# Performance work log

Measured on AMD Instinct MI355X. Metric: run time of the kernel, lower is better.

Reference implementation:

```python
import jax, jax.numpy as jnp
import numpy as np

H = 1024
NH = 16
HD = H // NH  # 64

def setup_inputs() -> dict:
    key = jax.random.key(0)
    ks = jax.random.split(key, 6)
    B, S = 2, 2048
    hidden_states = jax.random.normal(ks[0], (B, S, H), dtype=jnp.float32)
    attention_mask = jnp.ones((B, S), dtype=jnp.int32)
    sc = 1.0 / np.sqrt(H)
    Wq = jax.random.normal(ks[1], (H, H), dtype=jnp.float32) * sc
    Wk = jax.random.normal(ks[2], (H, H), dtype=jnp.float32) * sc
    Wv = jax.random.normal(ks[3], (H, H), dtype=jnp.float32) * sc
    Wo = jax.random.normal(ks[4], (H, H), dtype=jnp.float32) * sc
    return {"hidden_states": hidden_states, "attention_mask": attention_mask,
            "Wq": Wq, "Wk": Wk, "Wv": Wv, "Wo": Wo}

def reference(hidden_states, attention_mask, Wq, Wk, Wv, Wo):
    B, S, _ = hidden_states.shape
    # nn.Linear(bias=False): y = x @ W.T
    q = hidden_states @ Wq.T
    k = hidden_states @ Wk.T
    v = hidden_states @ Wv.T
    # [B, NH, S, HD]
    q = q.reshape(B, S, NH, HD).transpose(0, 2, 1, 3)
    k = k.reshape(B, S, NH, HD).transpose(0, 2, 1, 3)
    v = v.reshape(B, S, NH, HD).transpose(0, 2, 1, 3)
    # ELU+1 feature map
    q = jax.nn.elu(q) + 1.0
    k = jax.nn.elu(k) + 1.0
    # [B, NH, S, S]
    attn = jnp.einsum('bhqd,bhkd->bhqk', q, k)
    mask = attention_mask[:, None, None, :]  # [B,1,1,S]
    attn = jnp.where(mask == 0, -jnp.inf, attn)
    attn = jax.nn.softmax(attn, axis=-1)
    # dropout p=0.0 (eval) -> identity
    out = jnp.einsum('bhqk,bhkd->bhqd', attn, v)
    out = out.transpose(0, 2, 1, 3).reshape(B, S, H)
    return out @ Wo.T
```

## Files before the change

kernel.cpp:

```cpp
#include <hip/hip_runtime.h>

#define H_ 1024
#define NH_ 16
#define HD_ 64
#define B_ 2
#define S_ 2048
#define BS_ 4096

typedef _Float16 half8 __attribute__((ext_vector_type(8)));
typedef _Float16 half4_t __attribute__((ext_vector_type(4)));
typedef float floatx4 __attribute__((ext_vector_type(4)));

#define LOG2E 1.44269504088896f

__device__ __forceinline__ void async_copy16(void* lds, const void* g) {
  __builtin_amdgcn_global_load_lds(
      (const __attribute__((address_space(1))) unsigned int*)g,
      (__attribute__((address_space(3))) unsigned int*)lds, 16, 0, 0);
}

__global__ __launch_bounds__(256) void cvt_all(
    const float* __restrict__ hs, const float* __restrict__ wq,
    const float* __restrict__ wk, const float* __restrict__ wv,
    const float* __restrict__ wo,
    _Float16* __restrict__ hs_h, _Float16* __restrict__ w_h) {
  int i = blockIdx.x * 256 + threadIdx.x;
  int idx = i * 4;
  const float* src; _Float16* dst; int off;
  if (idx < BS_ * H_) {
    src = hs; dst = hs_h; off = idx;
  } else {
    int j = idx - BS_ * H_;
    int w = j >> 20;
    off = j & ((1 << 20) - 1);
    src = (w == 0) ? wq : (w == 1) ? wk : (w == 2) ? wv : wo;
    dst = w_h + (size_t)w * (H_ * H_);
  }
  float4 f = *(const float4*)(src + off);
  half4_t o;
  o.x = (_Float16)f.x; o.y = (_Float16)f.y;
  o.z = (_Float16)f.z; o.w = (_Float16)f.w;
  *(half4_t*)(dst + off) = o;
}

__global__ __launch_bounds__(256) void qkv_gemm(
    const _Float16* __restrict__ A, const _Float16* __restrict__ Wall,
    _Float16* __restrict__ qh, _Float16* __restrict__ kh,
    _Float16* __restrict__ vt) {
  const int z = blockIdx.z;
  const _Float16* W = Wall + (size_t)z * (H_ * H_);
  const int rbase = blockIdx.y * 128;
  const int cbase = blockIdx.x * 128;
  __shared__ _Float16 As[128 * 32];
  __shared__ _Float16 Bs[128 * 32];
  const int tid = threadIdx.x, lane = tid & 63, w = tid >> 6;
  const int quad = lane >> 4, l16 = lane & 15;
  const int wr = (w >> 1) * 64, wc = (w & 1) * 64;

  floatx4 zero = {0.f, 0.f, 0.f, 0.f};
  floatx4 acc[4][4];
#pragma unroll
  for (int i = 0; i < 4; ++i)
#pragma unroll
    for (int j = 0; j < 4; ++j) acc[i][j] = zero;

  const int srow = w * 32 + (lane >> 2);
  const int sseg = (lane & 3) * 8;
  const _Float16* Ag = A + (size_t)(rbase + srow) * H_ + sseg;
  const _Float16* Bg = W + (size_t)(cbase + srow) * H_ + sseg;

  for (int k0 = 0; k0 < H_; k0 += 32) {
    async_copy16(&As[(w * 32) * 32], Ag + k0);
    async_copy16(&As[(w * 32 + 16) * 32], Ag + 16 * H_ + k0);
    async_copy16(&Bs[(w * 32) * 32], Bg + k0);
    async_copy16(&Bs[(w * 32 + 16) * 32], Bg + 16 * H_ + k0);
    __syncthreads();
    half8 af[4], bf[4];
#pragma unroll
    for (int t = 0; t < 4; ++t)
      af[t] = *(half8*)&As[(wr + t * 16 + l16) * 32 + quad * 8];
#pragma unroll
    for (int t = 0; t < 4; ++t)
      bf[t] = *(half8*)&Bs[(wc + t * 16 + l16) * 32 + quad * 8];
#pragma unroll
    for (int i = 0; i < 4; ++i)
#pragma unroll
      for (int j = 0; j < 4; ++j)
        acc[i][j] = __builtin_amdgcn_mfma_f32_16x16x32_f16(af[i], bf[j],
                                                           acc[i][j], 0, 0, 0);
    __syncthreads();
  }
#pragma unroll
  for (int i = 0; i < 4; ++i) {
    int r0 = rbase + wr + i * 16 + quad * 4;
    int b = r0 >> 11, sl0 = r0 & (S_ - 1);
#pragma unroll
    for (int j = 0; j < 4; ++j) {
      int col = cbase + wc + j * 16 + l16;
      int h = col >> 6, d = col & 63;
      if (z == 2) {
        half4_t pk;
#pragma unroll
        for (int r = 0; r < 4; ++r) pk[r] = (_Float16)acc[i][j][r];
        *(half4_t*)&vt[((size_t)(b * NH_ + h) * HD_ + d) * S_ + sl0] = pk;
      } else {
        _Float16* outp = (z == 0) ? qh : kh;
        float scale = (z == 0) ? LOG2E : 1.0f;
#pragma unroll
        for (int r = 0; r < 4; ++r) {
          float x = acc[i][j][r];
          x = ((x > 0.f) ? (x + 1.f) : __expf(x)) * scale;
          outp[((size_t)(b * NH_ + h) * S_ + sl0 + r) * HD_ + d] = (_Float16)x;
        }
      }
    }
  }
}

__global__ __launch_bounds__(256, 2) void flash_attn(
    const _Float16* __restrict__ qh, const _Float16* __restrict__ kh,
    const _Float16* __restrict__ vt, const int* __restrict__ mask,
    _Float16* __restrict__ attn_out) {
  const int bh = blockIdx.y, b = bh >> 4, h = bh & 15;
  const int qbase = blockIdx.x * 128;
  const int tid = threadIdx.x, w = tid >> 6, lane = tid & 63;
  const int quad = lane >> 4, l16 = lane & 15;

  __shared__ _Float16 Kt[128 * 64];
  __shared__ _Float16 Vt[64 * 128];
  __shared__ _Float16 Pt[4][32 * 68];

  const _Float16* Q = qh + (size_t)bh * (S_ * HD_);
  const _Float16* K = kh + (size_t)bh * (S_ * HD_);
  const _Float16* Vg = vt + (size_t)bh * (HD_ * S_);
  const int* Mb = mask + b * S_;

  half8 qf[2][2];
#pragma unroll
  for (int g = 0; g < 2; ++g) {
    int qr = qbase + w * 32 + g * 16 + l16;
    qf[g][0] = *(const half8*)&Q[qr * 64 + quad * 8];
    qf[g][1] = *(const half8*)&Q[qr * 64 + 32 + quad * 8];
  }

  floatx4 zero = {0.f, 0.f, 0.f, 0.f};
  floatx4 o[2][4];
#pragma unroll
  for (int g = 0; g < 2; ++g)
#pragma unroll
    for (int i = 0; i < 4; ++i) o[g][i] = zero;
  float mi[2][4], li[2][4];
#pragma unroll
  for (int g = 0; g < 2; ++g)
#pragma unroll
    for (int r = 0; r < 4; ++r) { mi[g][r] = -3e38f; li[g][r] = 0.f; }

  const int krow_off = lane >> 3;
  const int kslot = lane & 7;
  const int kchunk = kslot ^ (krow_off & 7);
  const int vrow_off = lane >> 4;
  const int vslot = lane & 15;

  for (int kt = 0; kt < S_ / 128; ++kt) {
    const int key0 = kt * 128;
#pragma unroll
    for (int u = 0; u < 4; ++u) {
      int kl = w * 32 + u * 8;
      async_copy16(&Kt[kl * 64],
                   K + (size_t)(key0 + kl + krow_off) * 64 + kchunk * 8);
    }
#pragma unroll
    for (int u = 0; u < 4; ++u) {
      int d0 = w * 16 + u * 4 + vrow_off;
      int c0 = vslot ^ (d0 & 15);
      async_copy16(&Vt[(w * 16 + u * 4) * 128],
                   Vg + (size_t)d0 * S_ + key0 + c0 * 8);
    }
    int m0 = Mb[key0 + lane];
    int m1 = Mb[key0 + 64 + lane];
    __syncthreads();

    floatx4 sa[2][8];
#pragma unroll
    for (int g = 0; g < 2; ++g)
#pragma unroll
      for (int ct = 0; ct < 8; ++ct) sa[g][ct] = zero;
    {
      int s0 = quad ^ (l16 & 7);
      int s1 = (4 + quad) ^ (l16 & 7);
#pragma unroll
      for (int ct = 0; ct < 8; ++ct) {
        int key = ct * 16 + l16;
        half8 bf0 = *(half8*)&Kt[key * 64 + s0 * 8];
        half8 bf1 = *(half8*)&Kt[key * 64 + s1 * 8];
        sa[0][ct] = __builtin_amdgcn_mfma_f32_16x16x32_f16(qf[0][0], bf0, sa[0][ct], 0, 0, 0);
        sa[0][ct] = __builtin_amdgcn_mfma_f32_16x16x32_f16(qf[0][1], bf1, sa[0][ct], 0, 0, 0);
        sa[1][ct] = __builtin_amdgcn_mfma_f32_16x16x32_f16(qf[1][0], bf0, sa[1][ct], 0, 0, 0);
        sa[1][ct] = __builtin_amdgcn_mfma_f32_16x16x32_f16(qf[1][1], bf1, sa[1][ct], 0, 0, 0);
      }
    }
    if (__any((m0 == 0) || (m1 == 0))) {
#pragma unroll
      for (int ct = 0; ct < 8; ++ct) {
        if (Mb[key0 + ct * 16 + l16] == 0) {
#pragma unroll
          for (int g = 0; g < 2; ++g) {
            sa[g][ct][0] = -1e30f; sa[g][ct][1] = -1e30f;
            sa[g][ct][2] = -1e30f; sa[g][ct][3] = -1e30f;
          }
        }
      }
    }
#pragma unroll
    for (int g = 0; g < 2; ++g)
#pragma unroll
      for (int r = 0; r < 4; ++r) {
        float mx = sa[g][0][r];
#pragma unroll
        for (int ct = 1; ct < 8; ++ct) mx = fmaxf(mx, sa[g][ct][r]);
        mx = fmaxf(mx, __shfl_xor(mx, 1));
        mx = fmaxf(mx, __shfl_xor(mx, 2));
        mx = fmaxf(mx, __shfl_xor(mx, 4));
        mx = fmaxf(mx, __shfl_xor(mx, 8));
        float mn = fmaxf(mi[g][r], mx);
        float alpha = __builtin_amdgcn_exp2f(mi[g][r] - mn);
        mi[g][r] = mn;
        float rs = 0.f;
#pragma unroll
        for (int ct = 0; ct < 8; ++ct) {
          float p = __builtin_amdgcn_exp2f(sa[g][ct][r] - mn);
          sa[g][ct][r] = p;
          rs += p;
        }
        rs += __shfl_xor(rs, 1);
        rs += __shfl_xor(rs, 2);
        rs += __shfl_xor(rs, 4);
        rs += __shfl_xor(rs, 8);
        li[g][r] = li[g][r] * alpha + rs;
        o[g][0][r] *= alpha; o[g][1][r] *= alpha;
        o[g][2][r] *= alpha; o[g][3][r] *= alpha;
      }
#pragma unroll
    for (int hv = 0; hv < 2; ++hv) {
#pragma unroll
      for (int g = 0; g < 2; ++g)
#pragma unroll
        for (int c = 0; c < 4; ++c)
#pragma unroll
          for (int r = 0; r < 4; ++r)
            Pt[w][(g * 16 + quad * 4 + r) * 68 + c * 16 + l16] =
                (_Float16)sa[g][hv * 4 + c][r];
      __builtin_amdgcn_s_waitcnt(0xC07F);
#pragma unroll
      for (int kk2 = 0; kk2 < 2; ++kk2) {
        int kk = hv * 2 + kk2;
        half8 pf0 = *(half8*)&Pt[w][l16 * 68 + kk2 * 32 + quad * 8];
        half8 pf1 = *(half8*)&Pt[w][(16 + l16) * 68 + kk2 * 32 + quad * 8];
#pragma unroll
        for (int ct2 = 0; ct2 < 4; ++ct2) {
          int d = ct2 * 16 + l16;
          int vs = (kk * 4 + quad) ^ (l16 & 15);
          half8 vf = *(half8*)&Vt[d * 128 + vs * 8];
          o[0][ct2] = __builtin_amdgcn_mfma_f32_16x16x32_f16(pf0, vf, o[0][ct2], 0, 0, 0);
          o[1][ct2] = __builtin_amdgcn_mfma_f32_16x16x32_f16(pf1, vf, o[1][ct2], 0, 0, 0);
        }
      }
    }
    __syncthreads();
  }
#pragma unroll
  for (int g = 0; g < 2; ++g)
#pragma unroll
    for (int ct2 = 0; ct2 < 4; ++ct2)
#pragma unroll
      for (int r = 0; r < 4; ++r) {
        int row = qbase + w * 32 + g * 16 + quad * 4 + r;
        int d = ct2 * 16 + l16;
        float val = o[g][ct2][r] / li[g][r];
        attn_out[((size_t)(b * S_ + row)) * H_ + h * HD_ + d] = (_Float16)val;
      }
}

__global__ __launch_bounds__(256) void out_gemm(
    const _Float16* __restrict__ A, const _Float16* __restrict__ W,
    float* __restrict__ out) {
  const int rbase = blockIdx.y * 128;
  const int cbase = blockIdx.x * 64;
  __shared__ _Float16 As[128 * 32];
  __shared__ _Float16 Bs[64 * 32];
  const int tid = threadIdx.x, lane = tid & 63, w = tid >> 6;
  const int quad = lane >> 4, l16 = lane & 15;

  floatx4 zero = {0.f, 0.f, 0.f, 0.f};
  floatx4 acc[2][4];
#pragma unroll
  for (int i = 0; i < 2; ++i)
#pragma unroll
    for (int j = 0; j < 4; ++j) acc[i][j] = zero;

  const int srowA = w * 32 + (lane >> 2);
  const int srowB = w * 16 + (lane >> 2);
  const int sseg = (lane & 3) * 8;
  const _Float16* Ag = A + (size_t)(rbase + srowA) * H_ + sseg;
  const _Float16* Bg = W + (size_t)(cbase + srowB) * H_ + sseg;

  for (int k0 = 0; k0 < H_; k0 += 32) {
    async_copy16(&As[(w * 32) * 32], Ag + k0);
    async_copy16(&As[(w * 32 + 16) * 32], Ag + 16 * H_ + k0);
    async_copy16(&Bs[(w * 16) * 32], Bg + k0);
    __syncthreads();
    half8 af[2], bf[4];
#pragma unroll
    for (int t = 0; t < 2; ++t)
      af[t] = *(half8*)&As[(w * 32 + t * 16 + l16) * 32 + quad * 8];
#pragma unroll
    for (int t = 0; t < 4; ++t)
      bf[t] = *(half8*)&Bs[(t * 16 + l16) * 32 + quad * 8];
#pragma unroll
    for (int i = 0; i < 2; ++i)
#pragma unroll
      for (int j = 0; j < 4; ++j)
        acc[i][j] = __builtin_amdgcn_mfma_f32_16x16x32_f16(af[i], bf[j],
                                                           acc[i][j], 0, 0, 0);
    __syncthreads();
  }
#pragma unroll
  for (int i = 0; i < 2; ++i) {
    int r0 = rbase + w * 32 + i * 16 + quad * 4;
#pragma unroll
    for (int j = 0; j < 4; ++j) {
      int col = cbase + j * 16 + l16;
#pragma unroll
      for (int r = 0; r < 4; ++r)
        out[(size_t)(r0 + r) * H_ + col] = acc[i][j][r];
    }
  }
}

extern "C" void kernel_launch(void* const* d_in, const int* in_sizes, int n_in,
                              void* d_out, int out_size, void* d_ws,
                              size_t ws_size, hipStream_t stream) {
  const float* hs = (const float*)d_in[0];
  const int* mask = (const int*)d_in[1];
  const float* Wq = (const float*)d_in[2];
  const float* Wk = (const float*)d_in[3];
  const float* Wv = (const float*)d_in[4];
  const float* Wo = (const float*)d_in[5];
  float* out = (float*)d_out;

  _Float16* p = (_Float16*)d_ws;
  _Float16* hs_h = p; p += (size_t)BS_ * H_;
  _Float16* w_h = p;  p += (size_t)4 * H_ * H_;
  _Float16* q_h = p;  p += (size_t)BS_ * H_;
  _Float16* k_h = p;  p += (size_t)BS_ * H_;
  _Float16* v_t = p;  p += (size_t)BS_ * H_;
  _Float16* ao_h = p; p += (size_t)BS_ * H_;

  cvt_all<<<8192, 256, 0, stream>>>(hs, Wq, Wk, Wv, Wo, hs_h, w_h);
  qkv_gemm<<<dim3(8, 32, 3), 256, 0, stream>>>(hs_h, w_h, q_h, k_h, v_t);
  flash_attn<<<dim3(16, 32), 256, 0, stream>>>(q_h, k_h, v_t, mask, ao_h);
  out_gemm<<<dim3(16, 32), 256, 0, stream>>>(ao_h, w_h + (size_t)3 * H_ * H_, out);
}
```

Baseline: 213.9 us.

## Double-buffer K/V tiles and keep P in registers via transposed MFMA

The attention kernel now double-buffers K and V tiles in LDS, issuing the async load for the next tile before computing the current one, so there is one barrier per iteration. The QK^T MFMA operands are swapped so each lane holds a whole query row's scores. That lets the row max and sum use two cross-quad shuffles instead of four, and lets P be fed straight from registers into 16x16x16 MFMAs for PV, dropping the P round-trip through LDS. The output is written as packed half4 stores. The trade-off is twice the K/V LDS footprint, which may limit occupancy, and a smaller-K MFMA shape for the PV product.

New measurement: 192.7 us. 1.11x faster.

```diff
diff --git a/kernel.cpp b/kernel.cpp
--- a/kernel.cpp
+++ b/kernel.cpp
@@ -126,9 +126,8 @@
   const int tid = threadIdx.x, w = tid >> 6, lane = tid & 63;
   const int quad = lane >> 4, l16 = lane & 15;
 
-  __shared__ _Float16 Kt[128 * 64];
-  __shared__ _Float16 Vt[64 * 128];
-  __shared__ _Float16 Pt[4][32 * 68];
+  __shared__ _Float16 Kt[2][128 * 64];
+  __shared__ _Float16 Vt[2][64 * 128];
 
   const _Float16* Q = qh + (size_t)bh * (S_ * HD_);
   const _Float16* K = kh + (size_t)bh * (S_ * HD_);
@@ -149,11 +148,7 @@
   for (int g = 0; g < 2; ++g)
 #pragma unroll
     for (int i = 0; i < 4; ++i) o[g][i] = zero;
-  float mi[2][4], li[2][4];
-#pragma unroll
-  for (int g = 0; g < 2; ++g)
-#pragma unroll
-    for (int r = 0; r < 4; ++r) { mi[g][r] = -3e38f; li[g][r] = 0.f; }
+  float mi[2] = {-3e38f, -3e38f}, li[2] = {0.f, 0.f};
 
   const int krow_off = lane >> 3;
   const int kslot = lane & 7;
@@ -161,24 +156,45 @@
   const int vrow_off = lane >> 4;
   const int vslot = lane & 15;
 
-  for (int kt = 0; kt < S_ / 128; ++kt) {
-    const int key0 = kt * 128;
+  {
 #pragma unroll
     for (int u = 0; u < 4; ++u) {
       int kl = w * 32 + u * 8;
-      async_copy16(&Kt[kl * 64],
-                   K + (size_t)(key0 + kl + krow_off) * 64 + kchunk * 8);
+      async_copy16(&Kt[0][kl * 64], K + (size_t)(kl + krow_off) * 64 + kchunk * 8);
     }
 #pragma unroll
     for (int u = 0; u < 4; ++u) {
       int d0 = w * 16 + u * 4 + vrow_off;
       int c0 = vslot ^ (d0 & 15);
-      async_copy16(&Vt[(w * 16 + u * 4) * 128],
-                   Vg + (size_t)d0 * S_ + key0 + c0 * 8);
+      async_copy16(&Vt[0][(w * 16 + u * 4) * 128], Vg + (size_t)d0 * S_ + c0 * 8);
+    }
+  }
+
+  for (int kt = 0; kt < S_ / 128; ++kt) {
+    const int key0 = kt * 128;
+    const int buf = kt & 1;
+    __syncthreads();
+    if (kt < S_ / 128 - 1) {
+      const int key1 = key0 + 128;
+#pragma unroll
+      for (int u = 0; u < 4; ++u) {
+        int kl = w * 32 + u * 8;
+        async_copy16(&Kt[buf ^ 1][kl * 64],
+                     K + (size_t)(key1 + kl + krow_off) * 64 + kchunk * 8);
+      }
+#pragma unroll
+      for (int u = 0; u < 4; ++u) {
+        int d0 = w * 16 + u * 4 + vrow_off;
+        int c0 = vslot ^ (d0 & 15);
+        async_copy16(&Vt[buf ^ 1][(w * 16 + u * 4) * 128],
+                     Vg + (size_t)d0 * S_ + key1 + c0 * 8);
+      }
     }
     int m0 = Mb[key0 + lane];
     int m1 = Mb[key0 + 64 + lane];
-    __syncthreads();
+
+    const _Float16* Kb = &Kt[buf][0];
+    const _Float16* Vb = &Vt[buf][0];
 
     floatx4 sa[2][8];
 #pragma unroll
@@ -191,94 +207,86 @@
 #pragma unroll
       for (int ct = 0; ct < 8; ++ct) {
         int key = ct * 16 + l16;
-        half8 bf0 = *(half8*)&Kt[key * 64 + s0 * 8];
-        half8 bf1 = *(half8*)&Kt[key * 64 + s1 * 8];
-        sa[0][ct] = __builtin_amdgcn_mfma_f32_16x16x32_f16(qf[0][0], bf0, sa[0][ct], 0, 0, 0);
-        sa[0][ct] = __builtin_amdgcn_mfma_f32_16x16x32_f16(qf[0][1], bf1, sa[0][ct], 0, 0, 0);
-        sa[1][ct] = __builtin_amdgcn_mfma_f32_16x16x32_f16(qf[1][0], bf0, sa[1][ct], 0, 0, 0);
-        sa[1][ct] = __builtin_amdgcn_mfma_f32_16x16x32_f16(qf[1][1], bf1, sa[1][ct], 0, 0, 0);
+        half8 bf0 = *(half8*)&Kb[key * 64 + s0 * 8];
+        half8 bf1 = *(half8*)&Kb[key * 64 + s1 * 8];
+        sa[0][ct] = __builtin_amdgcn_mfma_f32_16x16x32_f16(bf0, qf[0][0], sa[0][ct], 0, 0, 0);
+        sa[0][ct] = __builtin_amdgcn_mfma_f32_16x16x32_f16(bf1, qf[0][1], sa[0][ct], 0, 0, 0);
+        sa[1][ct] = __builtin_amdgcn_mfma_f32_16x16x32_f16(bf0, qf[1][0], sa[1][ct], 0, 0, 0);
+        sa[1][ct] = __builtin_amdgcn_mfma_f32_16x16x32_f16(bf1, qf[1][1], sa[1][ct], 0, 0, 0);
       }
     }
     if (__any((m0 == 0) || (m1 == 0))) {
 #pragma unroll
-      for (int ct = 0; ct < 8; ++ct) {
-        if (Mb[key0 + ct * 16 + l16] == 0) {
-#pragma unroll
-          for (int g = 0; g < 2; ++g) {
-            sa[g][ct][0] = -1e30f; sa[g][ct][1] = -1e30f;
-            sa[g][ct][2] = -1e30f; sa[g][ct][3] = -1e30f;
+      for (int ct = 0; ct < 8; ++ct)
+#pragma unroll
+        for (int r = 0; r < 4; ++r)
+          if (Mb[key0 + ct * 16 + quad * 4 + r] == 0) {
+            sa[0][ct][r] = -1e30f;
+            sa[1][ct][r] = -1e30f;
           }
-        }
-      }
-    }
-#pragma unroll
-    for (int g = 0; g < 2; ++g)
-#pragma unroll
-      for (int r = 0; r < 4; ++r) {
-        float mx = sa[g][0][r];
-#pragma unroll
-        for (int ct = 1; ct < 8; ++ct) mx = fmaxf(mx, sa[g][ct][r]);
-        mx = fmaxf(mx, __shfl_xor(mx, 1));
-        mx = fmaxf(mx, __shfl_xor(mx, 2));
-        mx = fmaxf(mx, __shfl_xor(mx, 4));
-        mx = fmaxf(mx, __shfl_xor(mx, 8));
-        float mn = fmaxf(mi[g][r], mx);
-        float alpha = __builtin_amdgcn_exp2f(mi[g][r] - mn);
-        mi[g][r] = mn;
-        float rs = 0.f;
-#pragma unroll
-        for (int ct = 0; ct < 8; ++ct) {
+    }
+#pragma unroll
+    for (int g = 0; g < 2; ++g) {
+      float mx = sa[g][0][0];
+#pragma unroll
+      for (int ct = 0; ct < 8; ++ct)
+#pragma unroll
+        for (int r = 0; r < 4; ++r) mx = fmaxf(mx, sa[g][ct][r]);
+      mx = fmaxf(mx, __shfl_xor(mx, 16));
+      mx = fmaxf(mx, __shfl_xor(mx, 32));
+      float mn = fmaxf(mi[g], mx);
+      float alpha = __builtin_amdgcn_exp2f(mi[g] - mn);
+      mi[g] = mn;
+      float rs = 0.f;
+#pragma unroll
+      for (int ct = 0; ct < 8; ++ct)
+#pragma unroll
+        for (int r = 0; r < 4; ++r) {
           float p = __builtin_amdgcn_exp2f(sa[g][ct][r] - mn);
           sa[g][ct][r] = p;
           rs += p;
         }
-        rs += __shfl_xor(rs, 1);
-        rs += __shfl_xor(rs, 2);
-        rs += __shfl_xor(rs, 4);
-        rs += __shfl_xor(rs, 8);
-        li[g][r] = li[g][r] * alpha + rs;
-        o[g][0][r] *= alpha; o[g][1][r] *= alpha;
-        o[g][2][r] *= alpha; o[g][3][r] *= alpha;
-      }
-#pragma unroll
-    for (int hv = 0; hv < 2; ++hv) {
-#pragma unroll
-      for (int g = 0; g < 2; ++g)
-#pragma unroll
-        for (int c = 0; c < 4; ++c)
-#pragma unroll
-          for (int r = 0; r < 4; ++r)
-            Pt[w][(g * 16 + quad * 4 + r) * 68 + c * 16 + l16] =
-                (_Float16)sa[g][hv * 4 + c][r];
-      __builtin_amdgcn_s_waitcnt(0xC07F);
-#pragma unroll
-      for (int kk2 = 0; kk2 < 2; ++kk2) {
-        int kk = hv * 2 + kk2;
-        half8 pf0 = *(half8*)&Pt[w][l16 * 68 + kk2 * 32 + quad * 8];
-        half8 pf1 = *(half8*)&Pt[w][(16 + l16) * 68 + kk2 * 32 + quad * 8];
-#pragma unroll
-        for (int ct2 = 0; ct2 < 4; ++ct2) {
-          int d = ct2 * 16 + l16;
-          int vs = (kk * 4 + quad) ^ (l16 & 15);
-          half8 vf = *(half8*)&Vt[d * 128 + vs * 8];
-          o[0][ct2] = __builtin_amdgcn_mfma_f32_16x16x32_f16(pf0, vf, o[0][ct2], 0, 0, 0);
-          o[1][ct2] = __builtin_amdgcn_mfma_f32_16x16x32_f16(pf1, vf, o[1][ct2], 0, 0, 0);
-        }
-      }
-    }
-    __syncthreads();
-  }
-#pragma unroll
-  for (int g = 0; g < 2; ++g)
-#pragma unroll
-    for (int ct2 = 0; ct2 < 4; ++ct2)
+      rs += __shfl_xor(rs, 16);
+      rs += __shfl_xor(rs, 32);
+      li[g] = li[g] * alpha + rs;
+#pragma unroll
+      for (int ct2 = 0; ct2 < 4; ++ct2) {
+        o[g][ct2][0] *= alpha; o[g][ct2][1] *= alpha;
+        o[g][ct2][2] *= alpha; o[g][ct2][3] *= alpha;
+      }
+    }
+#pragma unroll
+    for (int ct = 0; ct < 8; ++ct) {
+      half4_t p0, p1;
 #pragma unroll
       for (int r = 0; r < 4; ++r) {
-        int row = qbase + w * 32 + g * 16 + quad * 4 + r;
+        p0[r] = (_Float16)sa[0][ct][r];
+        p1[r] = (_Float16)sa[1][ct][r];
+      }
+      int chunk = (2 * ct + (quad >> 1)) ^ l16;
+      int off = chunk * 8 + (quad & 1) * 4;
+#pragma unroll
+      for (int ct2 = 0; ct2 < 4; ++ct2) {
         int d = ct2 * 16 + l16;
-        float val = o[g][ct2][r] / li[g][r];
-        attn_out[((size_t)(b * S_ + row)) * H_ + h * HD_ + d] = (_Float16)val;
-      }
+        half4_t vf = *(half4_t*)&Vb[d * 128 + off];
+        o[0][ct2] = __builtin_amdgcn_mfma_f32_16x16x16f16(vf, p0, o[0][ct2], 0, 0, 0);
+        o[1][ct2] = __builtin_amdgcn_mfma_f32_16x16x16f16(vf, p1, o[1][ct2], 0, 0, 0);
+      }
+    }
+  }
+#pragma unroll
+  for (int g = 0; g < 2; ++g) {
+    float inv = 1.0f / li[g];
+    int row = qbase + w * 32 + g * 16 + l16;
+#pragma unroll
+    for (int ct2 = 0; ct2 < 4; ++ct2) {
+      half4_t pk;
+#pragma unroll
+      for (int r = 0; r < 4; ++r) pk[r] = (_Float16)(o[g][ct2][r] * inv);
+      int d = ct2 * 16 + quad * 4;
+      *(half4_t*)&attn_out[((size_t)(b * S_ + row)) * H_ + h * HD_ + d] = pk;
+    }
+  }
 }
 
 __global__ __launch_bounds__(256) void out_gemm(
```
